# Performance work log

Measured on AMD Instinct MI355X. Metric: run time of the kernel, lower is better.

Reference implementation:

```python
import jax, jax.numpy as jnp
import numpy as np

EPS = 1e-5
D_MODEL = 128; D_INNER = 256; D_STATE = 64; D_CONV = 4; NHEADS = 8; HEADDIM = 32
N_LAYERS = 4; PATCH = 16; IMG = 512; BATCH = 16
D_IN_PROJ = 2 * D_INNER + 2 * D_STATE + NHEADS  # 648
CONV_DIM = D_INNER + 2 * D_STATE               # 384


def _layernorm(x, g, b):
    m = jnp.mean(x, -1, keepdims=True)
    v = jnp.mean((x - m) ** 2, -1, keepdims=True)
    return (x - m) * jax.lax.rsqrt(v + EPS) * g + b


def _mamba2(x, in_w, conv_w, conv_b, dt_bias, A_log, D_skip, norm_w, out_w):
    # x: (b, l, d_model). Faithful to mamba-ssm Mamba2 (ngroups=1, rmsnorm gated, D skip).
    b, l, _ = x.shape
    zxbcdt = jnp.einsum('bld,ed->ble', x, in_w)            # (b,l,648)
    z = zxbcdt[..., :D_INNER]
    xBC = zxbcdt[..., D_INNER:D_INNER + CONV_DIM]
    dt = zxbcdt[..., -NHEADS:]
    # causal depthwise conv1d (kernel D_CONV) + SiLU
    xpad = jnp.pad(xBC, ((0, 0), (D_CONV - 1, 0), (0, 0)))
    xc = conv_b + sum(xpad[:, k:k + l, :] * conv_w[:, k] for k in range(D_CONV))
    xc = jax.nn.silu(xc)
    xs = xc[..., :D_INNER]
    B = xc[..., D_INNER:D_INNER + D_STATE]                 # (b,l,n)
    C = xc[..., -D_STATE:]                                 # (b,l,n)
    dt = jax.nn.softplus(dt + dt_bias)                     # (b,l,h)
    dA = jnp.exp(dt * (-jnp.exp(A_log)))                   # (b,l,h)
    xh = xs.reshape(b, l, NHEADS, HEADDIM)                 # (b,l,h,p)

    def step(hstate, t):
        dA_t, dt_t, B_t, x_t, C_t = t
        hstate = hstate * dA_t[:, :, None, None] + jnp.einsum('bh,bn,bhp->bhpn', dt_t, B_t, x_t)
        return hstate, jnp.einsum('bhpn,bn->bhp', hstate, C_t)

    h0 = jnp.zeros((b, NHEADS, HEADDIM, D_STATE), x.dtype)
    _, ys = jax.lax.scan(step, h0, (dA.swapaxes(0, 1), dt.swapaxes(0, 1), B.swapaxes(0, 1), xh.swapaxes(0, 1), C.swapaxes(0, 1)))
    y = ys.swapaxes(0, 1) + D_skip[None, None, :, None] * xh
    y = y.reshape(b, l, D_INNER)
    y = y * jax.nn.silu(z)                                 # gate
    y = y * jax.lax.rsqrt(jnp.mean(y * y, -1, keepdims=True) + EPS) * norm_w  # gated RMSNorm
    return jnp.einsum('ble,de->bld', y, out_w)


def _forward(x, patch_w, patch_b, pe_g, pe_b, in_w, conv_w, conv_b, dt_bias, A_log,
             D_skip, ssm_norm_w, out_w, ln_g, ln_b, fn_g, fn_b, attn_w1, attn_b1, attn_w2, attn_b2):
    b = x.shape[0]
    Hp = x.shape[2] // PATCH; Wp = x.shape[3] // PATCH
    # patch-embed conv (stride==kernel) as a reshape + einsum
    xp = x.reshape(b, 3, Hp, PATCH, Wp, PATCH)
    tok = jnp.einsum('bchpwq,dcpq->bhwd', xp, patch_w) + patch_b
    tok = tok.reshape(b, Hp * Wp, D_MODEL)
    tok = _layernorm(tok, pe_g, pe_b)
    for i in range(N_LAYERS):
        res = tok
        tok = _layernorm(tok, ln_g[i], ln_b[i])
        tok = _mamba2(tok, in_w[i], conv_w[i], conv_b[i], dt_bias[i], A_log[i],
                      D_skip[i], ssm_norm_w[i], out_w[i])
        tok = tok + res
    tok = _layernorm(tok, fn_g, fn_b)
    # attention pooling
    h1 = jnp.tanh(jnp.einsum('bld,hd->blh', tok, attn_w1) + attn_b1)
    scores = jnp.einsum('blh,oh->blo', h1, attn_w2) + attn_b2
    w = jax.nn.softmax(scores, axis=1)
    pooled = jnp.sum(w * tok, axis=1)
    nrm = jnp.maximum(jnp.sqrt(jnp.sum(pooled * pooled, -1, keepdims=True)), 1e-12)
    return pooled / nrm


def setup_inputs() -> dict:
    key = jax.random.key(0)
    ks = jax.random.split(key, 16)
    n = lambda k, shape, s=0.02: (jax.random.normal(k, shape) * s).astype(jnp.float32)
    return {
        'x': jax.random.normal(ks[0], (BATCH, 3, IMG, IMG), jnp.float32),
        'patch_w': n(ks[1], (D_MODEL, 3, PATCH, PATCH)),
        'patch_b': jnp.zeros((D_MODEL,), jnp.float32),
        'pe_g': jnp.ones((D_MODEL,), jnp.float32),
        'pe_b': jnp.zeros((D_MODEL,), jnp.float32),
        'in_w': n(ks[2], (N_LAYERS, D_IN_PROJ, D_MODEL)),
        'conv_w': n(ks[3], (N_LAYERS, CONV_DIM, D_CONV), 0.1),
        'conv_b': jnp.zeros((N_LAYERS, CONV_DIM), jnp.float32),
        'dt_bias': n(ks[4], (N_LAYERS, NHEADS), 0.5),
        'A_log': jnp.log(jax.random.uniform(ks[5], (N_LAYERS, NHEADS), jnp.float32, 1.0, 16.0)),
        'D_skip': jnp.ones((N_LAYERS, NHEADS), jnp.float32),
        'ssm_norm_w': jnp.ones((N_LAYERS, D_INNER), jnp.float32),
        'out_w': n(ks[6], (N_LAYERS, D_MODEL, D_INNER)),
        'ln_g': jnp.ones((N_LAYERS, D_MODEL), jnp.float32),
        'ln_b': jnp.zeros((N_LAYERS, D_MODEL), jnp.float32),
        'fn_g': jnp.ones((D_MODEL,), jnp.float32),
        'fn_b': jnp.zeros((D_MODEL,), jnp.float32),
        'attn_w1': n(ks[7], (D_MODEL // 2, D_MODEL), 0.05),
        'attn_b1': jnp.zeros((D_MODEL // 2,), jnp.float32),
        'attn_w2': n(ks[8], (1, D_MODEL // 2), 0.05),
        'attn_b2': jnp.zeros((1,), jnp.float32),
    }


def reference(x, patch_w, patch_b, pe_g, pe_b, in_w, conv_w, conv_b, dt_bias, A_log,
              D_skip, ssm_norm_w, out_w, ln_g, ln_b, fn_g, fn_b, attn_w1, attn_b1, attn_w2, attn_b2):
    return _forward(x, patch_w, patch_b, pe_g, pe_b, in_w, conv_w, conv_b, dt_bias, A_log,
                    D_skip, ssm_norm_w, out_w, ln_g, ln_b, fn_g, fn_b, attn_w1, attn_b1, attn_w2, attn_b2)
```

## Files before the change

### kernel.cpp

```cpp
#include <hip/hip_runtime.h>
#include <math.h>

#define EPS 1e-5f

constexpr int NB      = 16;
constexpr int L       = 1024;
constexpr int DM      = 128;
constexpr int DI      = 256;
constexpr int DS      = 64;
constexpr int NH      = 8;
constexpr int DPROJ   = 648;
constexpr int CDIM    = 384;
constexpr int EPAD    = 656;

typedef __attribute__((ext_vector_type(8))) short short8v;
typedef __attribute__((ext_vector_type(4))) float f32x4;
typedef unsigned short ushort_t;

__device__ __forceinline__ float silu_f(float x){ return x / (1.f + expf(-x)); }
__device__ __forceinline__ ushort_t f2bf(float f){
  union { float f; unsigned int u; } v; v.f = f;
  unsigned int r = v.u + 0x7FFF + ((v.u >> 16) & 1);
  return (ushort_t)(r >> 16);
}
__device__ __forceinline__ short8v pack8(float4 a, float4 b){
  short8v v;
  v[0]=(short)f2bf(a.x); v[1]=(short)f2bf(a.y); v[2]=(short)f2bf(a.z); v[3]=(short)f2bf(a.w);
  v[4]=(short)f2bf(b.x); v[5]=(short)f2bf(b.y); v[6]=(short)f2bf(b.z); v[7]=(short)f2bf(b.w);
  return v;
}

__global__ __launch_bounds__(256) void k_cvt(const float* __restrict__ in_w,
    const float* __restrict__ ln_g, const float* __restrict__ ln_b,
    const float* __restrict__ out_w, const float* __restrict__ nw,
    const float* __restrict__ patch_w, const float* __restrict__ w1,
    ushort_t* __restrict__ inwb, ushort_t* __restrict__ owb,
    ushort_t* __restrict__ pwb, float* __restrict__ biasin,
    ushort_t* __restrict__ w1b){
  const int R1 = 4 * EPAD * 128, R2 = 4 * 128 * 256, R3 = 128 * 768, R4 = 4 * EPAD, R5 = 64 * 128;
  int i = blockIdx.x * 256 + threadIdx.x;
  if (i < R1) {
    int ly = i / (EPAD * 128), rem = i % (EPAD * 128), e = rem >> 7, d = rem & 127;
    float v = 0.f;
    if (e < DPROJ) v = in_w[((size_t)ly * DPROJ + e) * 128 + d] * ln_g[ly * 128 + d];
    inwb[i] = f2bf(v);
    return;
  }
  i -= R1;
  if (i < R2) {
    int ly = i >> 15, rem = i & 32767, e = rem & 255;
    owb[i] = f2bf(out_w[i] * nw[ly * 256 + e]);
    return;
  }
  i -= R2;
  if (i < R3) { pwb[i] = f2bf(patch_w[i]); return; }
  i -= R3;
  if (i < R4) {
    int ly = i / EPAD, e = i % EPAD;
    float s = 0.f;
    if (e < DPROJ) {
      const float* r = in_w + ((size_t)ly * DPROJ + e) * 128;
      const float* b = ln_b + ly * 128;
      for (int d = 0; d < 128; ++d) s += r[d] * b[d];
    }
    biasin[i] = s;
    return;
  }
  i -= R4;
  if (i < R5) w1b[i] = f2bf(w1[i]);
}

__global__ __launch_bounds__(256) void k_patch(const float* __restrict__ x,
    const ushort_t* __restrict__ pwb, const float* __restrict__ pb,
    const float* __restrict__ pg, const float* __restrict__ pbe,
    float* __restrict__ tok){
  __shared__ ushort_t Al[64 * 128];
  __shared__ ushort_t Bl[128 * 128];
  __shared__ float spb[128], spg[128], spe[128];
  const int m0 = blockIdx.x * 64;
  const int tid = threadIdx.x;
  char* Ab = (char*)Al; char* Bb = (char*)Bl;
  if (tid < 128) { spb[tid] = pb[tid]; spg[tid] = pg[tid]; spe[tid] = pbe[tid]; }
  const int w = tid >> 6, l = tid & 63, lr = l & 15, lgp = l >> 4;
  f32x4 acc[8];
#pragma unroll
  for (int nt = 0; nt < 8; ++nt) acc[nt] = (f32x4){0.f, 0.f, 0.f, 0.f};
  for (int kc = 0; kc < 6; ++kc) {
    __syncthreads();
    for (int idx = tid; idx < 128 * 16; idx += 256) {
      int n = idx >> 4, ch = idx & 15;
      short8v v = *(const short8v*)(pwb + (size_t)n * 768 + kc * 128 + (ch << 3));
      *(short8v*)(Bb + n * 256 + ((ch * 16) ^ ((n & 7) << 4))) = v;
    }
    {
      const int c = kc >> 1;
      for (int i = tid; i < 1024; i += 256) {
        int t = i >> 4, p = (i >> 1) & 7, o = i & 1;
        int T = m0 + t, bb = T >> 10, tl = T & 1023, hp = tl >> 5, wp = tl & 31;
        const float* src = x + (((size_t)(bb * 3 + c) * 512 + hp * 16 + ((kc & 1) << 3) + p) * 512
                                + wp * 16 + o * 8);
        float4 f0 = *(const float4*)src;
        float4 f1 = *(const float4*)(src + 4);
        short8v v = pack8(f0, f1);
        int kk = p * 16 + o * 8;
        *(short8v*)(Ab + t * 256 + ((kk * 2) ^ ((t & 7) << 4))) = v;
      }
    }
    __syncthreads();
    short8v a[4];
#pragma unroll
    for (int ks = 0; ks < 4; ++ks)
      a[ks] = *(const short8v*)(Ab + (16 * w + lr) * 256 + ((ks * 64 + lgp * 16) ^ ((lr & 7) << 4)));
#pragma unroll
    for (int nt = 0; nt < 8; ++nt) {
#pragma unroll
      for (int ks = 0; ks < 4; ++ks) {
        short8v b = *(const short8v*)(Bb + (nt * 16 + lr) * 256 + ((ks * 64 + lgp * 16) ^ ((lr & 7) << 4)));
        acc[nt] = __builtin_amdgcn_mfma_f32_16x16x32_bf16(a[ks], b, acc[nt], 0, 0, 0);
      }
    }
  }
  float s4[4] = {0,0,0,0}, q4[4] = {0,0,0,0};
#pragma unroll
  for (int nt = 0; nt < 8; ++nt) {
    const float bb = spb[nt * 16 + lr];
#pragma unroll
    for (int r = 0; r < 4; ++r) { float v = acc[nt][r] + bb; s4[r] += v; q4[r] += v * v; }
  }
#pragma unroll
  for (int r = 0; r < 4; ++r) {
    for (int off = 1; off < 16; off <<= 1) {
      s4[r] += __shfl_xor(s4[r], off, 16);
      q4[r] += __shfl_xor(q4[r], off, 16);
    }
  }
#pragma unroll
  for (int r = 0; r < 4; ++r) {
    float mean = s4[r] * (1.f / 128.f);
    float var  = q4[r] * (1.f / 128.f) - mean * mean;
    float rstd = rsqrtf(var + EPS);
    const size_t row = (size_t)(m0 + 16 * w + lgp * 4 + r) * 128;
#pragma unroll
    for (int nt = 0; nt < 8; ++nt) {
      int col = nt * 16 + lr;
      float v = acc[nt][r] + spb[col];
      tok[row + col] = (v - mean) * rstd * spg[col] + spe[col];
    }
  }
}

__global__ __launch_bounds__(256) void k_inproj(const float* __restrict__ tok,
    const ushort_t* __restrict__ inwb, const float* __restrict__ biasin,
    float* __restrict__ zx){
  __shared__ ushort_t Al[128 * 128];
  __shared__ ushort_t Bl[176 * 128];
  __shared__ float sBias[176];
  const int blk = blockIdx.x;
  const int mb = blk >> 2, nb = blk & 3;
  const int m0 = mb << 7, n0 = nb * 176;
  const int NT = (nb == 3) ? 128 : 176;
  const int tid = threadIdx.x;
  char* Ab = (char*)Al; char* Bb = (char*)Bl;
  for (int idx = tid; idx < (NT << 4); idx += 256) {
    int row = idx >> 4, ch = idx & 15;
    short8v v = *(const short8v*)(inwb + ((size_t)(n0 + row) << 7) + (ch << 3));
    *(short8v*)(Bb + row * 256 + ((ch * 16) ^ ((row & 7) << 4))) = v;
  }
  for (int idx = tid; idx < NT; idx += 256) sBias[idx] = biasin[n0 + idx];
  for (int rp = 0; rp < 2; ++rp) {
    const int r = (rp << 6) + (tid >> 2), t4 = tid & 3;
    const float* src = tok + (((size_t)(m0 + r)) << 7) + t4 * 32;
    float v[32];
    float s = 0.f, sq = 0.f;
#pragma unroll
    for (int k = 0; k < 8; ++k) {
      float4 f = *(const float4*)(src + 4 * k);
      v[4*k] = f.x; v[4*k+1] = f.y; v[4*k+2] = f.z; v[4*k+3] = f.w;
      s += f.x + f.y + f.z + f.w;
      sq += f.x*f.x + f.y*f.y + f.z*f.z + f.w*f.w;
    }
    s  += __shfl_xor(s, 1, 4);  s  += __shfl_xor(s, 2, 4);
    sq += __shfl_xor(sq, 1, 4); sq += __shfl_xor(sq, 2, 4);
    float mean = s * (1.f / 128.f);
    float var  = sq * (1.f / 128.f) - mean * mean;
    float rstd = rsqrtf(var + EPS);
#pragma unroll
    for (int k = 0; k < 4; ++k) {
      short8v o;
#pragma unroll
      for (int e = 0; e < 8; ++e) o[e] = (short)f2bf((v[8*k + e] - mean) * rstd);
      *(short8v*)(Ab + r * 256 + ((t4 * 64 + 16 * k) ^ ((r & 7) << 4))) = o;
    }
  }
  __syncthreads();
  const int w = tid >> 6, l = tid & 63, lr = l & 15, lgp = l >> 4;
  const int xsl = (lr & 7) << 4;
  short8v a[2][4];
#pragma unroll
  for (int mi = 0; mi < 2; ++mi) {
    const int mt = w + mi * 4;
#pragma unroll
    for (int ks = 0; ks < 4; ++ks)
      a[mi][ks] = *(const short8v*)(Ab + (16 * mt + lr) * 256 + ((ks * 64 + lgp * 16) ^ xsl));
  }
  const int NTT = NT >> 4;
  for (int nt = 0; nt < NTT; ++nt) {
    f32x4 acc0 = (f32x4){0.f, 0.f, 0.f, 0.f};
    f32x4 acc1 = (f32x4){0.f, 0.f, 0.f, 0.f};
#pragma unroll
    for (int ks = 0; ks < 4; ++ks) {
      short8v b = *(const short8v*)(Bb + (nt * 16 + lr) * 256 + ((ks * 64 + lgp * 16) ^ xsl));
      acc0 = __builtin_amdgcn_mfma_f32_16x16x32_bf16(a[0][ks], b, acc0, 0, 0, 0);
      acc1 = __builtin_amdgcn_mfma_f32_16x16x32_bf16(a[1][ks], b, acc1, 0, 0, 0);
    }
    const int col = n0 + nt * 16 + lr;
    if (col < DPROJ) {
      const float bias = sBias[nt * 16 + lr];
#pragma unroll
      for (int r = 0; r < 4; ++r) {
        zx[((size_t)(m0 + 16 * w       + lgp * 4 + r)) * DPROJ + col] = acc0[r] + bias;
        zx[((size_t)(m0 + 16 * (w + 4) + lgp * 4 + r)) * DPROJ + col] = acc1[r] + bias;
      }
    }
  }
}

constexpr int CONVC = 192;
__global__ __launch_bounds__(256) void k_conv(const float* __restrict__ zx,
    const float* __restrict__ cw, const float* __restrict__ cb, float* __restrict__ xc){
  __shared__ float st[67][CONVC];
  __shared__ float swt[CONVC][4];
  __shared__ float sbias[CONVC];
  const int blk = blockIdx.x;
  const int cg = blk & 1, tile = (blk >> 1) & 15, b = blk >> 5;
  const int l0 = tile << 6, ch0 = cg * CONVC;
  const int tid = threadIdx.x;
  for (int i = tid; i < CONVC; i += 256) {
    float4 wv = *(const float4*)(cw + (size_t)(ch0 + i) * 4);
    swt[i][0] = wv.x; swt[i][1] = wv.y; swt[i][2] = wv.z; swt[i][3] = wv.w;
    sbias[i] = cb[ch0 + i];
  }
  for (int i = tid; i < 67 * 48; i += 256) {
    int rr = i / 48, q4 = i % 48;
    int lrow = l0 + rr - 3;
    float4 v = make_float4(0.f, 0.f, 0.f, 0.f);
    if (lrow >= 0) v = *(const float4*)(zx + ((size_t)(b << 10) + lrow) * DPROJ + DI + ch0 + q4 * 4);
    *(float4*)(&st[rr][q4 * 4]) = v;
  }
  __syncthreads();
  for (int i = tid; i < 64 * CONVC; i += 256) {
    int t = i / CONVC, c2 = i % CONVC;
    float acc = sbias[c2] + st[t][c2] * swt[c2][0] + st[t+1][c2] * swt[c2][1]
              + st[t+2][c2] * swt[c2][2] + st[t+3][c2] * swt[c2][3];
    acc = silu_f(acc);
    xc[((size_t)(b << 10) + l0 + t) * CDIM + ch0 + c2] = acc;
  }
}

__global__ __launch_bounds__(64) void k_dt(const float* __restrict__ zx,
    const float* __restrict__ dtbias, const float* __restrict__ Alog,
    float* __restrict__ dtb, float* __restrict__ lcb, float* __restrict__ Acb){
  const int blk = blockIdx.x;
  const int c = blk & 15, h = (blk >> 4) & 7, b = blk >> 7;
  const int s = threadIdx.x;
  const int l = (c << 6) + s;
  float raw = zx[((size_t)(b << 10) + l) * DPROJ + 640 + h] + dtbias[h];
  float dt = raw > 20.f ? raw : log1pf(expf(raw));
  float la = dt * (-expf(Alog[h]));
  float cum = la;
  for (int off = 1; off < 64; off <<= 1) {
    float v = __shfl_up(cum, off, 64);
    if (s >= off) cum += v;
  }
  size_t o = ((size_t)((b << 3) + h) << 10) + l;
  dtb[o] = dt; lcb[o] = cum;
  if (s == 63) Acb[blk] = expf(cum);
}

__global__ __launch_bounds__(256) void k_cstate(const float* __restrict__ xc,
    const float* __restrict__ dtb, const float* __restrict__ lcb,
    float* __restrict__ Sc){
  __shared__ ushort_t sXc[32 * 64];
  __shared__ ushort_t sBt[64 * 64];
  __shared__ float scoef[64];
  const int blk = blockIdx.x;
  const int c = blk & 15, h = (blk >> 4) & 7, b = blk >> 7;
  const int tid = threadIdx.x;
  const int l0 = c << 6;
  char* pA = (char*)sXc; char* pB = (char*)sBt;
  const size_t obh = ((size_t)((b << 3) + h) << 10) + l0;
  if (tid < 64) {
    float lcT = lcb[obh + 63];
    scoef[tid] = dtb[obh + tid] * __expf(fminf(lcT - lcb[obh + tid], 0.f));
  }
  const int s = tid >> 2, q = tid & 3;
  const size_t rowb = ((size_t)(b << 10) + l0 + s) * CDIM;
  float4 b0 = *(const float4*)(xc + rowb + DI + q * 16);
  float4 b1 = *(const float4*)(xc + rowb + DI + q * 16 + 4);
  float4 b2 = *(const float4*)(xc + rowb + DI + q * 16 + 8);
  float4 b3 = *(const float4*)(xc + rowb + DI + q * 16 + 12);
  float4 x0 = *(const float4*)(xc + rowb + (h << 5) + q * 8);
  float4 x1 = *(const float4*)(xc + rowb + (h << 5) + q * 8 + 4);
  float bv[16] = {b0.x,b0.y,b0.z,b0.w, b1.x,b1.y,b1.z,b1.w,
                  b2.x,b2.y,b2.z,b2.w, b3.x,b3.y,b3.z,b3.w};
#pragma unroll
  for (int j = 0; j < 16; ++j) {
    const int n = q * 16 + j;
    *(ushort_t*)(pB + n * 128 + ((s * 2) ^ ((n & 7) << 4))) = f2bf(bv[j]);
  }
  __syncthreads();
  const float cf = scoef[s];
  float xv[8] = {x0.x,x0.y,x0.z,x0.w, x1.x,x1.y,x1.z,x1.w};
#pragma unroll
  for (int j = 0; j < 8; ++j) {
    const int p = q * 8 + j;
    *(ushort_t*)(pA + p * 128 + ((s * 2) ^ ((p & 7) << 4))) = f2bf(cf * xv[j]);
  }
  __syncthreads();
  const int w = tid >> 6, l = tid & 63, lr = l & 15, lgp = l >> 4;
  const int xsl = (lr & 7) << 4;
  const int pt = w & 1, ng = w >> 1;
  short8v a0 = *(const short8v*)(pA + (pt * 16 + lr) * 128 + ((lgp * 16) ^ xsl));
  short8v a1 = *(const short8v*)(pA + (pt * 16 + lr) * 128 + ((64 + lgp * 16) ^ xsl));
  float* dst = Sc + ((size_t)blk << 11);
#pragma unroll
  for (int ni = 0; ni < 2; ++ni) {
    const int nt = ng * 2 + ni;
    f32x4 acc = (f32x4){0.f, 0.f, 0.f, 0.f};
    short8v bb0 = *(const short8v*)(pB + (nt * 16 + lr) * 128 + ((lgp * 16) ^ xsl));
    short8v bb1 = *(const short8v*)(pB + (nt * 16 + lr) * 128 + ((64 + lgp * 16) ^ xsl));
    acc = __builtin_amdgcn_mfma_f32_16x16x32_bf16(a0, bb0, acc, 0, 0, 0);
    acc = __builtin_amdgcn_mfma_f32_16x16x32_bf16(a1, bb1, acc, 0, 0, 0);
#pragma unroll
    for (int r = 0; r < 4; ++r)
      dst[(pt * 16 + lgp * 4 + r) * 64 + nt * 16 + lr] = acc[r];
  }
}

__global__ __launch_bounds__(256) void k_hscan(float* __restrict__ Sc, const float* __restrict__ Acb){
  const int blk = blockIdx.x;
  const int bh = blk >> 3;
  const int e = ((blk & 7) << 8) + threadIdx.x;
  float hs = 0.f;
  const size_t base = ((size_t)bh << 15) + e;
  for (int c = 0; c < 16; ++c) {
    const size_t o = base + ((size_t)c << 11);
    float v = Sc[o];
    Sc[o] = hs;
    hs = Acb[(bh << 4) + c] * hs + v;
  }
}

__global__ __launch_bounds__(256) void k_chunky(const float* __restrict__ xc,
    const float* __restrict__ h0buf, const float* __restrict__ dtb,
    const float* __restrict__ lcb, const float* __restrict__ Dsk,
    float* __restrict__ ys){
  __shared__ ushort_t sC[64 * 64];
  __shared__ ushort_t sBm[64 * 64];
  __shared__ ushort_t sAW[64 * 128];
  __shared__ ushort_t sBX[32 * 128];
  __shared__ float sXT[32][65];
  __shared__ float sdt[64], slc[64];
  const int blk = blockIdx.x;
  const int c = blk & 15, h = (blk >> 4) & 7, b = blk >> 7;
  const int tid = threadIdx.x;
  const int l0 = c << 6;
  char* pC = (char*)sC; char* pB = (char*)sBm; char* pA = (char*)sAW; char* pX = (char*)sBX;
  const size_t obh = ((size_t)((b << 3) + h) << 10) + l0;
  if (tid < 64) { sdt[tid] = dtb[obh + tid]; slc[tid] = lcb[obh + tid]; }
  {
    const int row = tid >> 2, q = tid & 3;
    const size_t rowb = ((size_t)(b << 10) + l0 + row) * CDIM;
    const float Pt = __expf(lcb[obh + row]);
    const int xs = (row & 7) << 4;
    float4 b0 = *(const float4*)(xc + rowb + DI + q * 16);
    float4 b1 = *(const float4*)(xc + rowb + DI + q * 16 + 4);
    float4 b2 = *(const float4*)(xc + rowb + DI + q * 16 + 8);
    float4 b3 = *(const float4*)(xc + rowb + DI + q * 16 + 12);
    *(short8v*)(pB + row * 128 + ((q * 32) ^ xs))      = pack8(b0, b1);
    *(short8v*)(pB + row * 128 + ((q * 32 + 16) ^ xs)) = pack8(b2, b3);
    float4 c0 = *(const float4*)(xc + rowb + DI + DS + q * 16);
    float4 c1 = *(const float4*)(xc + rowb + DI + DS + q * 16 + 4);
    float4 c2 = *(const float4*)(xc + rowb + DI + DS + q * 16 + 8);
    float4 c3 = *(const float4*)(xc + rowb + DI + DS + q * 16 + 12);
    *(short8v*)(pC + row * 128 + ((q * 32) ^ xs))      = pack8(c0, c1);
    *(short8v*)(pC + row * 128 + ((q * 32 + 16) ^ xs)) = pack8(c2, c3);
    float4 p0 = make_float4(c0.x*Pt, c0.y*Pt, c0.z*Pt, c0.w*Pt);
    float4 p1 = make_float4(c1.x*Pt, c1.y*Pt, c1.z*Pt, c1.w*Pt);
    float4 p2 = make_float4(c2.x*Pt, c2.y*Pt, c2.z*Pt, c2.w*Pt);
    float4 p3 = make_float4(c3.x*Pt, c3.y*Pt, c3.z*Pt, c3.w*Pt);
    *(short8v*)(pA + row * 256 + ((128 + q * 32) ^ xs))      = pack8(p0, p1);
    *(short8v*)(pA + row * 256 + ((128 + q * 32 + 16) ^ xs)) = pack8(p2, p3);
    float4 x0 = *(const float4*)(xc + rowb + (h << 5) + q * 8);
    float4 x1 = *(const float4*)(xc + rowb + (h << 5) + q * 8 + 4);
    sXT[q*8+0][row] = x0.x; sXT[q*8+1][row] = x0.y; sXT[q*8+2][row] = x0.z; sXT[q*8+3][row] = x0.w;
    sXT[q*8+4][row] = x1.x; sXT[q*8+5][row] = x1.y; sXT[q*8+6][row] = x1.z; sXT[q*8+7][row] = x1.w;
  }
  {
    const int p = tid >> 3, n8 = (tid & 7) << 3;
    float4 h0a = *(const float4*)(h0buf + ((size_t)blk << 11) + (p << 6) + n8);
    float4 h0b = *(const float4*)(h0buf + ((size_t)blk << 11) + (p << 6) + n8 + 4);
    *(short8v*)(pX + p * 256 + (((64 + n8) * 2) ^ ((p & 7) << 4))) = pack8(h0a, h0b);
  }
  __syncthreads();
  {
    const int p = tid >> 3, s8 = (tid & 7) << 3;
    short8v vx;
#pragma unroll
    for (int e = 0; e < 8; ++e) vx[e] = (short)f2bf(sXT[p][s8 + e]);
    *(short8v*)(pX + p * 256 + ((s8 * 2) ^ ((p & 7) << 4))) = vx;
  }
  const int w = tid >> 6, l = tid & 63, lr = l & 15, lgp = l >> 4;
  const int xsl = (lr & 7) << 4;
  f32x4 accg[4];
#pragma unroll
  for (int nt = 0; nt < 4; ++nt) accg[nt] = (f32x4){0.f, 0.f, 0.f, 0.f};
  {
    short8v a0 = *(const short8v*)(pC + (16 * w + lr) * 128 + ((lgp * 16) ^ xsl));
    short8v a1 = *(const short8v*)(pC + (16 * w + lr) * 128 + ((64 + lgp * 16) ^ xsl));
#pragma unroll
    for (int nt = 0; nt < 4; ++nt) {
      short8v b0 = *(const short8v*)(pB + (nt * 16 + lr) * 128 + ((lgp * 16) ^ xsl));
      short8v b1 = *(const short8v*)(pB + (nt * 16 + lr) * 128 + ((64 + lgp * 16) ^ xsl));
      accg[nt] = __builtin_amdgcn_mfma_f32_16x16x32_bf16(a0, b0, accg[nt], 0, 0, 0);
      accg[nt] = __builtin_amdgcn_mfma_f32_16x16x32_bf16(a1, b1, accg[nt], 0, 0, 0);
    }
  }
#pragma unroll
  for (int nt = 0; nt < 4; ++nt) {
    const int s = nt * 16 + lr;
    const float ds = sdt[s], ls = slc[s];
#pragma unroll
    for (int r = 0; r < 4; ++r) {
      const int t = 16 * w + lgp * 4 + r;
      float wv = 0.f;
      if (s <= t) wv = ds * __expf(fminf(slc[t] - ls, 0.f)) * accg[nt][r];
      *(ushort_t*)(pA + t * 256 + ((s * 2) ^ ((t & 7) << 4))) = f2bf(wv);
    }
  }
  __syncthreads();
  f32x4 accy[2];
  accy[0] = (f32x4){0.f, 0.f, 0.f, 0.f};
  accy[1] = (f32x4){0.f, 0.f, 0.f, 0.f};
  short8v aw[4];
#pragma unroll
  for (int ks = 0; ks < 4; ++ks)
    aw[ks] = *(const short8v*)(pA + (16 * w + lr) * 256 + ((ks * 64 + lgp * 16) ^ xsl));
#pragma unroll
  for (int nt = 0; nt < 2; ++nt) {
#pragma unroll
    for (int ks = 0; ks < 4; ++ks) {
      short8v bx = *(const short8v*)(pX + (nt * 16 + lr) * 256 + ((ks * 64 + lgp * 16) ^ xsl));
      accy[nt] = __builtin_amdgcn_mfma_f32_16x16x32_bf16(aw[ks], bx, accy[nt], 0, 0, 0);
    }
  }
  const float dsk = Dsk[h];
#pragma unroll
  for (int nt = 0; nt < 2; ++nt) {
    const int p = nt * 16 + lr;
#pragma unroll
    for (int r = 0; r < 4; ++r) {
      const int t = 16 * w + lgp * 4 + r;
      ys[((size_t)(b << 10) + l0 + t) * DI + (h << 5) + p] = accy[nt][r] + dsk * sXT[p][t];
    }
  }
}

__global__ __launch_bounds__(256) void k_gateout(const float* __restrict__ zx,
    const float* __restrict__ ys, const ushort_t* __restrict__ owb,
    float* __restrict__ tok){
  __shared__ ushort_t Al[64 * 256];
  __shared__ ushort_t Bl[128 * 64];
  const int m0 = blockIdx.x * 64;
  const int tid = threadIdx.x;
  char* Ab = (char*)Al; char* Bb = (char*)Bl;
  {
    const int r = tid >> 2, t4 = tid & 3;
    const size_t row = (size_t)(m0 + r);
    const float* yp = ys + row * 256 + t4 * 64;
    const float* zp = zx + row * DPROJ + t4 * 64;
    float p[64];
    float sq = 0.f;
#pragma unroll
    for (int k = 0; k < 16; ++k) {
      float4 fy = *(const float4*)(yp + 4 * k);
      float4 fz = *(const float4*)(zp + 4 * k);
      float a0 = fy.x * (fz.x / (1.f + __expf(-fz.x)));
      float a1 = fy.y * (fz.y / (1.f + __expf(-fz.y)));
      float a2 = fy.z * (fz.z / (1.f + __expf(-fz.z)));
      float a3 = fy.w * (fz.w / (1.f + __expf(-fz.w)));
      p[4*k] = a0; p[4*k+1] = a1; p[4*k+2] = a2; p[4*k+3] = a3;
      sq += a0*a0 + a1*a1 + a2*a2 + a3*a3;
    }
    sq += __shfl_xor(sq, 1, 4); sq += __shfl_xor(sq, 2, 4);
    float rstd = rsqrtf(sq * (1.f / 256.f) + EPS);
#pragma unroll
    for (int k = 0; k < 8; ++k) {
      short8v o;
#pragma unroll
      for (int e = 0; e < 8; ++e) o[e] = (short)f2bf(p[8*k + e] * rstd);
      *(short8v*)(Ab + r * 512 + ((t4 * 128 + 16 * k) ^ ((r & 7) << 4))) = o;
    }
  }
  const int w = tid >> 6, l = tid & 63, lr = l & 15, lgp = l >> 4;
  f32x4 acc[8];
#pragma unroll
  for (int nt = 0; nt < 8; ++nt) acc[nt] = (f32x4){0.f, 0.f, 0.f, 0.f};
  for (int kq = 0; kq < 4; ++kq) {
    __syncthreads();
    for (int idx = tid; idx < 128 * 8; idx += 256) {
      int row = idx >> 3, ch = idx & 7;
      short8v v = *(const short8v*)(owb + ((size_t)row << 8) + kq * 64 + (ch << 3));
      *(short8v*)(Bb + row * 128 + ((ch * 16) ^ ((row & 7) << 4))) = v;
    }
    __syncthreads();
    short8v a0 = *(const short8v*)(Ab + (16*w + lr) * 512 + ((kq * 128 +      lgp * 16) ^ ((lr & 7) << 4)));
    short8v a1 = *(const short8v*)(Ab + (16*w + lr) * 512 + ((kq * 128 + 64 + lgp * 16) ^ ((lr & 7) << 4)));
#pragma unroll
    for (int nt = 0; nt < 8; ++nt) {
      short8v b0 = *(const short8v*)(Bb + (nt * 16 + lr) * 128 + ((     lgp * 16) ^ ((lr & 7) << 4)));
      short8v b1 = *(const short8v*)(Bb + (nt * 16 + lr) * 128 + ((64 + lgp * 16) ^ ((lr & 7) << 4)));
      acc[nt] = __builtin_amdgcn_mfma_f32_16x16x32_bf16(a0, b0, acc[nt], 0, 0, 0);
      acc[nt] = __builtin_amdgcn_mfma_f32_16x16x32_bf16(a1, b1, acc[nt], 0, 0, 0);
    }
  }
#pragma unroll
  for (int nt = 0; nt < 8; ++nt) {
#pragma unroll
    for (int r = 0; r < 4; ++r) {
      tok[((size_t)(m0 + 16 * w + lgp * 4 + r)) * 128 + nt * 16 + lr] += acc[nt][r];
    }
  }
}

__global__ __launch_bounds__(256) void k_score(const float* __restrict__ tok,
    const float* __restrict__ fg, const float* __restrict__ fb,
    const ushort_t* __restrict__ w1b, const float* __restrict__ b1,
    const float* __restrict__ w2, const float* __restrict__ b2,
    float* __restrict__ tokF, float* __restrict__ sc){
  __shared__ ushort_t Al[64 * 128];
  __shared__ ushort_t Wl[64 * 128];
  __shared__ float sb1[64], sw2[64];
  const int m0 = blockIdx.x * 64;
  const int tid = threadIdx.x;
  char* Ab = (char*)Al; char* Wb = (char*)Wl;
  for (int idx = tid; idx < 64 * 16; idx += 256) {
    int row = idx >> 4, ch = idx & 15;
    short8v v = *(const short8v*)(w1b + (row << 7) + (ch << 3));
    *(short8v*)(Wb + row * 256 + ((ch * 16) ^ ((row & 7) << 4))) = v;
  }
  if (tid < 64) { sb1[tid] = b1[tid]; sw2[tid] = w2[tid]; }
  {
    const int r = tid >> 2, t4 = tid & 3;
    const float* src = tok + (((size_t)(m0 + r)) << 7) + t4 * 32;
    float v[32];
    float s = 0.f, sq = 0.f;
#pragma unroll
    for (int k = 0; k < 8; ++k) {
      float4 f = *(const float4*)(src + 4 * k);
      v[4*k] = f.x; v[4*k+1] = f.y; v[4*k+2] = f.z; v[4*k+3] = f.w;
      s += f.x + f.y + f.z + f.w;
      sq += f.x*f.x + f.y*f.y + f.z*f.z + f.w*f.w;
    }
    s  += __shfl_xor(s, 1, 4);  s  += __shfl_xor(s, 2, 4);
    sq += __shfl_xor(sq, 1, 4); sq += __shfl_xor(sq, 2, 4);
    float mean = s * (1.f / 128.f);
    float var  = sq * (1.f / 128.f) - mean * mean;
    float rstd = rsqrtf(var + EPS);
    float* tdst = tokF + (((size_t)(m0 + r)) << 7) + t4 * 32;
#pragma unroll
    for (int k = 0; k < 4; ++k) {
      float o8[8];
      float4 g0 = *(const float4*)(fg + t4 * 32 + 8 * k);
      float4 g1 = *(const float4*)(fg + t4 * 32 + 8 * k + 4);
      float4 e0 = *(const float4*)(fb + t4 * 32 + 8 * k);
      float4 e1 = *(const float4*)(fb + t4 * 32 + 8 * k + 4);
      o8[0] = (v[8*k+0]-mean)*rstd*g0.x + e0.x; o8[1] = (v[8*k+1]-mean)*rstd*g0.y + e0.y;
      o8[2] = (v[8*k+2]-mean)*rstd*g0.z + e0.z; o8[3] = (v[8*k+3]-mean)*rstd*g0.w + e0.w;
      o8[4] = (v[8*k+4]-mean)*rstd*g1.x + e1.x; o8[5] = (v[8*k+5]-mean)*rstd*g1.y + e1.y;
      o8[6] = (v[8*k+6]-mean)*rstd*g1.z + e1.z; o8[7] = (v[8*k+7]-mean)*rstd*g1.w + e1.w;
      *(float4*)(tdst + 8*k)     = make_float4(o8[0], o8[1], o8[2], o8[3]);
      *(float4*)(tdst + 8*k + 4) = make_float4(o8[4], o8[5], o8[6], o8[7]);
      short8v ov;
#pragma unroll
      for (int e = 0; e < 8; ++e) ov[e] = (short)f2bf(o8[e]);
      *(short8v*)(Ab + r * 256 + ((t4 * 64 + 16 * k) ^ ((r & 7) << 4))) = ov;
    }
  }
  __syncthreads();
  const int w = tid >> 6, l = tid & 63, lr = l & 15, lgp = l >> 4;
  const int xsl = (lr & 7) << 4;
  short8v a[4];
#pragma unroll
  for (int ks = 0; ks < 4; ++ks)
    a[ks] = *(const short8v*)(Ab + (16 * w + lr) * 256 + ((ks * 64 + lgp * 16) ^ xsl));
  float sacc[4] = {0.f, 0.f, 0.f, 0.f};
#pragma unroll
  for (int nt = 0; nt < 4; ++nt) {
    f32x4 acc = (f32x4){0.f, 0.f, 0.f, 0.f};
#pragma unroll
    for (int ks = 0; ks < 4; ++ks) {
      short8v bb = *(const short8v*)(Wb + (nt * 16 + lr) * 256 + ((ks * 64 + lgp * 16) ^ xsl));
      acc = __builtin_amdgcn_mfma_f32_16x16x32_bf16(a[ks], bb, acc, 0, 0, 0);
    }
    const float bias = sb1[nt * 16 + lr], wv = sw2[nt * 16 + lr];
#pragma unroll
    for (int r = 0; r < 4; ++r) sacc[r] += tanhf(acc[r] + bias) * wv;
  }
#pragma unroll
  for (int r = 0; r < 4; ++r) {
    for (int off = 1; off < 16; off <<= 1) sacc[r] += __shfl_xor(sacc[r], off, 16);
  }
  if (lr == 0) {
    const float bb2 = b2[0];
#pragma unroll
    for (int r = 0; r < 4; ++r) sc[m0 + 16 * w + lgp * 4 + r] = sacc[r] + bb2;
  }
}

__global__ __launch_bounds__(256) void k_pool1(const float* __restrict__ tokF,
    const float* __restrict__ sc, float* __restrict__ pp){
  __shared__ float sw[128];
  __shared__ float sacc[128];
  __shared__ float sse[2];
  const int bs = blockIdx.x, b = bs >> 3, seg = bs & 7, tid = threadIdx.x;
  const int l0 = (b << 10) + (seg << 7);
  if (tid < 128) sw[tid] = __expf(sc[l0 + tid]);
  __syncthreads();
  const int d = tid & 127, g = tid >> 7;
  const float* tf = tokF + ((size_t)(l0 + (g << 6))) * 128 + d;
  float acc = 0.f;
#pragma unroll 4
  for (int i = 0; i < 64; ++i) acc += sw[(g << 6) + i] * tf[(size_t)i * 128];
  if (g == 0) sacc[d] = acc;
  float e = (tid < 128) ? sw[tid] : 0.f;
  for (int off = 32; off; off >>= 1) e += __shfl_xor(e, off);
  if ((tid & 63) == 0 && tid < 128) sse[tid >> 6] = e;
  __syncthreads();
  if (g == 1) pp[bs * 132 + d] = sacc[d] + acc;
  if (tid == 0) pp[bs * 132 + 128] = sse[0] + sse[1];
}

__global__ __launch_bounds__(128) void k_pool2(const float* __restrict__ pp,
    float* __restrict__ out){
  __shared__ float s2[2];
  const int b = blockIdx.x, tid = threadIdx.x;
  float num = 0.f, den = 0.f;
#pragma unroll
  for (int seg = 0; seg < 8; ++seg) {
    num += pp[(b * 8 + seg) * 132 + tid];
    den += pp[(b * 8 + seg) * 132 + 128];
  }
  float pooled = num / den;
  float sq = pooled * pooled;
  for (int off = 32; off; off >>= 1) sq += __shfl_xor(sq, off);
  if ((tid & 63) == 0) s2[tid >> 6] = sq;
  __syncthreads();
  float nrm = fmaxf(sqrtf(s2[0] + s2[1]), 1e-12f);
  out[(size_t)b * 128 + tid] = pooled / nrm;
}

extern "C" void kernel_launch(void* const* d_in, const int* in_sizes, int n_in,
                              void* d_out, int out_size, void* d_ws, size_t ws_size,
                              hipStream_t stream) {
  const float* x       = (const float*)d_in[0];
  const float* patch_w = (const float*)d_in[1];
  const float* patch_b = (const float*)d_in[2];
  const float* pe_g    = (const float*)d_in[3];
  const float* pe_b    = (const float*)d_in[4];
  const float* in_w    = (const float*)d_in[5];
  const float* conv_w  = (const float*)d_in[6];
  const float* conv_b  = (const float*)d_in[7];
  const float* dt_bias = (const float*)d_in[8];
  const float* A_log   = (const float*)d_in[9];
  const float* D_skip  = (const float*)d_in[10];
  const float* nw      = (const float*)d_in[11];
  const float* out_w   = (const float*)d_in[12];
  const float* ln_g    = (const float*)d_in[13];
  const float* ln_b    = (const float*)d_in[14];
  const float* fn_g    = (const float*)d_in[15];
  const float* fn_b    = (const float*)d_in[16];
  const float* w1      = (const float*)d_in[17];
  const float* b1      = (const float*)d_in[18];
  const float* w2      = (const float*)d_in[19];
  const float* b2      = (const float*)d_in[20];
  float* out = (float*)d_out;
  char* ws = (char*)d_ws;

  size_t off = 0;
  float* tok  = (float*)(ws + off); off += (size_t)NB * L * DM * 4;
  float* zx   = (float*)(ws + off); off += (size_t)NB * L * DPROJ * 4;
  float* xcb  = (float*)(ws + off); off += (size_t)NB * L * CDIM * 4;
  float* ysb  = (float*)(ws + off); off += (size_t)NB * L * DI * 4;
  float* Scb  = (float*)(ws + off); off += (size_t)NB * NH * 16 * 2048 * 4;
  float* dtb  = (float*)(ws + off); off += (size_t)NB * NH * L * 4;
  float* lcb  = (float*)(ws + off); off += (size_t)NB * NH * L * 4;
  float* Acb  = (float*)(ws + off); off += (size_t)NB * NH * 16 * 4;
  ushort_t* inwb = (ushort_t*)(ws + off); off += (size_t)4 * EPAD * 128 * 2;
  ushort_t* owb  = (ushort_t*)(ws + off); off += (size_t)4 * 128 * 256 * 2;
  ushort_t* pwb  = (ushort_t*)(ws + off); off += (size_t)128 * 768 * 2;
  float* biasin  = (float*)(ws + off); off += (size_t)4 * EPAD * 4;
  ushort_t* w1b  = (ushort_t*)(ws + off); off += (size_t)64 * 128 * 2;
  float* pp      = (float*)(ws + off); off += (size_t)128 * 132 * 4;
  float* tokF = zx;
  float* scb  = (float*)(ws + (size_t)30 * 1024 * 1024);

  {
    const int total = 4 * EPAD * 128 + 4 * 128 * 256 + 128 * 768 + 4 * EPAD + 64 * 128;
    k_cvt<<<(total + 255) / 256, 256, 0, stream>>>(in_w, ln_g, ln_b, out_w, nw, patch_w, w1,
                                                   inwb, owb, pwb, biasin, w1b);
  }
  k_patch<<<256, 256, 0, stream>>>(x, pwb, patch_b, pe_g, pe_b, tok);
  for (int ly = 0; ly < 4; ++ly) {
    k_inproj<<<512, 256, 0, stream>>>(tok, inwb + (size_t)ly * EPAD * 128,
                                      biasin + ly * EPAD, zx);
    k_conv<<<NB * 16 * 2, 256, 0, stream>>>(zx, conv_w + (size_t)ly * CDIM * 4,
                                            conv_b + ly * CDIM, xcb);
    k_dt<<<NB * NH * 16, 64, 0, stream>>>(zx, dt_bias + ly * NH, A_log + ly * NH,
                                          dtb, lcb, Acb);
    k_cstate<<<NB * NH * 16, 256, 0, stream>>>(xcb, dtb, lcb, Scb);
    k_hscan<<<NB * NH * 8, 256, 0, stream>>>(Scb, Acb);
    k_chunky<<<NB * NH * 16, 256, 0, stream>>>(xcb, Scb, dtb, lcb,
                                               D_skip + ly * NH, ysb);
    k_gateout<<<256, 256, 0, stream>>>(zx, ysb, owb + (size_t)ly * 128 * 256, tok);
  }
  k_score<<<256, 256, 0, stream>>>(tok, fn_g, fn_b, w1b, b1, w2, b2, tokF, scb);
  k_pool1<<<128, 256, 0, stream>>>(tokF, scb, pp);
  k_pool2<<<16, 128, 0, stream>>>(pp, out);
}
```

Before: 513.8 us.

## Store conv output and SSM output as bf16; fuse dt scan into conv kernel

The conv output (xc) and chunked-scan output (ys) buffers are now stored as bf16 instead of fp32, which halves their global memory traffic. Downstream kernels (cstate, chunky, gateout) read them as packed short8 vectors and convert where needed. The separate dt/softplus/cumsum kernel is folded into the conv kernel, so one launch per layer goes away. In exchange, precision is lower: xc is rounded to bf16 earlier, and the D-skip term plus the gate inputs now see bf16-rounded values.

```diff
diff --git a/kernel.cpp b/kernel.cpp
--- a/kernel.cpp
+++ b/kernel.cpp
@@ -14,6 +14,7 @@
 constexpr int EPAD    = 656;
 
 typedef __attribute__((ext_vector_type(8))) short short8v;
+typedef __attribute__((ext_vector_type(4))) short short4v;
 typedef __attribute__((ext_vector_type(4))) float f32x4;
 typedef unsigned short ushort_t;
 
@@ -22,6 +23,10 @@
   union { float f; unsigned int u; } v; v.f = f;
   unsigned int r = v.u + 0x7FFF + ((v.u >> 16) & 1);
   return (ushort_t)(r >> 16);
+}
+__device__ __forceinline__ float bf2f(ushort_t u){
+  union { float f; unsigned int u; } v; v.u = ((unsigned int)u) << 16;
+  return v.f;
 }
 __device__ __forceinline__ short8v pack8(float4 a, float4 b){
   short8v v;
@@ -227,7 +232,10 @@
 
 constexpr int CONVC = 192;
 __global__ __launch_bounds__(256) void k_conv(const float* __restrict__ zx,
-    const float* __restrict__ cw, const float* __restrict__ cb, float* __restrict__ xc){
+    const float* __restrict__ cw, const float* __restrict__ cb,
+    const float* __restrict__ dtbias, const float* __restrict__ Alog,
+    ushort_t* __restrict__ xc, float* __restrict__ dtb,
+    float* __restrict__ lcb, float* __restrict__ Acb){
   __shared__ float st[67][CONVC];
   __shared__ float swt[CONVC][4];
   __shared__ float sbias[CONVC];
@@ -247,37 +255,39 @@
     if (lrow >= 0) v = *(const float4*)(zx + ((size_t)(b << 10) + lrow) * DPROJ + DI + ch0 + q4 * 4);
     *(float4*)(&st[rr][q4 * 4]) = v;
   }
-  __syncthreads();
-  for (int i = tid; i < 64 * CONVC; i += 256) {
-    int t = i / CONVC, c2 = i % CONVC;
-    float acc = sbias[c2] + st[t][c2] * swt[c2][0] + st[t+1][c2] * swt[c2][1]
-              + st[t+2][c2] * swt[c2][2] + st[t+3][c2] * swt[c2][3];
-    acc = silu_f(acc);
-    xc[((size_t)(b << 10) + l0 + t) * CDIM + ch0 + c2] = acc;
-  }
-}
-
-__global__ __launch_bounds__(64) void k_dt(const float* __restrict__ zx,
-    const float* __restrict__ dtbias, const float* __restrict__ Alog,
-    float* __restrict__ dtb, float* __restrict__ lcb, float* __restrict__ Acb){
-  const int blk = blockIdx.x;
-  const int c = blk & 15, h = (blk >> 4) & 7, b = blk >> 7;
-  const int s = threadIdx.x;
-  const int l = (c << 6) + s;
-  float raw = zx[((size_t)(b << 10) + l) * DPROJ + 640 + h] + dtbias[h];
-  float dt = raw > 20.f ? raw : log1pf(expf(raw));
-  float la = dt * (-expf(Alog[h]));
-  float cum = la;
-  for (int off = 1; off < 64; off <<= 1) {
-    float v = __shfl_up(cum, off, 64);
-    if (s >= off) cum += v;
-  }
-  size_t o = ((size_t)((b << 3) + h) << 10) + l;
-  dtb[o] = dt; lcb[o] = cum;
-  if (s == 63) Acb[blk] = expf(cum);
-}
-
-__global__ __launch_bounds__(256) void k_cstate(const float* __restrict__ xc,
+  if (cg == 0) {
+    const int wv = tid >> 6, lane = tid & 63;
+#pragma unroll
+    for (int i = 0; i < 2; ++i) {
+      const int hh = wv * 2 + i;
+      float raw = zx[((size_t)(b << 10) + l0 + lane) * DPROJ + 640 + hh] + dtbias[hh];
+      float dt = raw > 20.f ? raw : log1pf(expf(raw));
+      float cum = dt * (-expf(Alog[hh]));
+      for (int off = 1; off < 64; off <<= 1) {
+        float v = __shfl_up(cum, off, 64);
+        if (lane >= off) cum += v;
+      }
+      size_t o = ((size_t)((b << 3) + hh) << 10) + l0 + lane;
+      dtb[o] = dt; lcb[o] = cum;
+      if (lane == 63) Acb[((b << 3) + hh) * 16 + tile] = expf(cum);
+    }
+  }
+  __syncthreads();
+  for (int i = tid; i < 64 * 48; i += 256) {
+    int t = i / 48, g = i % 48;
+    short4v ov;
+#pragma unroll
+    for (int j = 0; j < 4; ++j) {
+      int c2 = g * 4 + j;
+      float acc = sbias[c2] + st[t][c2] * swt[c2][0] + st[t+1][c2] * swt[c2][1]
+                + st[t+2][c2] * swt[c2][2] + st[t+3][c2] * swt[c2][3];
+      ov[j] = (short)f2bf(silu_f(acc));
+    }
+    *(short4v*)(xc + ((size_t)(b << 10) + l0 + t) * CDIM + ch0 + g * 4) = ov;
+  }
+}
+
+__global__ __launch_bounds__(256) void k_cstate(const ushort_t* __restrict__ xc,
     const float* __restrict__ dtb, const float* __restrict__ lcb,
     float* __restrict__ Sc){
   __shared__ ushort_t sXc[32 * 64];
@@ -294,27 +304,22 @@
     scoef[tid] = dtb[obh + tid] * __expf(fminf(lcT - lcb[obh + tid], 0.f));
   }
   const int s = tid >> 2, q = tid & 3;
-  const size_t rowb = ((size_t)(b << 10) + l0 + s) * CDIM;
-  float4 b0 = *(const float4*)(xc + rowb + DI + q * 16);
-  float4 b1 = *(const float4*)(xc + rowb + DI + q * 16 + 4);
-  float4 b2 = *(const float4*)(xc + rowb + DI + q * 16 + 8);
-  float4 b3 = *(const float4*)(xc + rowb + DI + q * 16 + 12);
-  float4 x0 = *(const float4*)(xc + rowb + (h << 5) + q * 8);
-  float4 x1 = *(const float4*)(xc + rowb + (h << 5) + q * 8 + 4);
-  float bv[16] = {b0.x,b0.y,b0.z,b0.w, b1.x,b1.y,b1.z,b1.w,
-                  b2.x,b2.y,b2.z,b2.w, b3.x,b3.y,b3.z,b3.w};
+  const ushort_t* xr = xc + ((size_t)(b << 10) + l0 + s) * CDIM;
+  short8v b0 = *(const short8v*)(xr + 256 + q * 16);
+  short8v b1 = *(const short8v*)(xr + 256 + q * 16 + 8);
+  short8v x8 = *(const short8v*)(xr + (h << 5) + q * 8);
 #pragma unroll
   for (int j = 0; j < 16; ++j) {
     const int n = q * 16 + j;
-    *(ushort_t*)(pB + n * 128 + ((s * 2) ^ ((n & 7) << 4))) = f2bf(bv[j]);
+    ushort_t bv = (ushort_t)(j < 8 ? b0[j] : b1[j - 8]);
+    *(ushort_t*)(pB + n * 128 + ((s * 2) ^ ((n & 7) << 4))) = bv;
   }
   __syncthreads();
   const float cf = scoef[s];
-  float xv[8] = {x0.x,x0.y,x0.z,x0.w, x1.x,x1.y,x1.z,x1.w};
 #pragma unroll
   for (int j = 0; j < 8; ++j) {
     const int p = q * 8 + j;
-    *(ushort_t*)(pA + p * 128 + ((s * 2) ^ ((p & 7) << 4))) = f2bf(cf * xv[j]);
+    *(ushort_t*)(pA + p * 128 + ((s * 2) ^ ((p & 7) << 4))) = f2bf(cf * bf2f((ushort_t)x8[j]));
   }
   __syncthreads();
   const int w = tid >> 6, l = tid & 63, lr = l & 15, lgp = l >> 4;
@@ -351,10 +356,10 @@
   }
 }
 
-__global__ __launch_bounds__(256) void k_chunky(const float* __restrict__ xc,
+__global__ __launch_bounds__(256) void k_chunky(const ushort_t* __restrict__ xc,
     const float* __restrict__ h0buf, const float* __restrict__ dtb,
     const float* __restrict__ lcb, const float* __restrict__ Dsk,
-    float* __restrict__ ys){
+    ushort_t* __restrict__ ys){
   __shared__ ushort_t sC[64 * 64];
   __shared__ ushort_t sBm[64 * 64];
   __shared__ ushort_t sAW[64 * 128];
@@ -370,31 +375,28 @@
   if (tid < 64) { sdt[tid] = dtb[obh + tid]; slc[tid] = lcb[obh + tid]; }
   {
     const int row = tid >> 2, q = tid & 3;
-    const size_t rowb = ((size_t)(b << 10) + l0 + row) * CDIM;
+    const ushort_t* xr = xc + ((size_t)(b << 10) + l0 + row) * CDIM;
+    const int xs = (row & 7) << 4;
+    short8v b0 = *(const short8v*)(xr + 256 + q * 16);
+    short8v b1 = *(const short8v*)(xr + 256 + q * 16 + 8);
+    *(short8v*)(pB + row * 128 + ((q * 32) ^ xs))      = b0;
+    *(short8v*)(pB + row * 128 + ((q * 32 + 16) ^ xs)) = b1;
+    short8v c0 = *(const short8v*)(xr + 320 + q * 16);
+    short8v c1 = *(const short8v*)(xr + 320 + q * 16 + 8);
+    *(short8v*)(pC + row * 128 + ((q * 32) ^ xs))      = c0;
+    *(short8v*)(pC + row * 128 + ((q * 32 + 16) ^ xs)) = c1;
     const float Pt = __expf(lcb[obh + row]);
-    const int xs = (row & 7) << 4;
-    float4 b0 = *(const float4*)(xc + rowb + DI + q * 16);
-    float4 b1 = *(const float4*)(xc + rowb + DI + q * 16 + 4);
-    float4 b2 = *(const float4*)(xc + rowb + DI + q * 16 + 8);
-    float4 b3 = *(const float4*)(xc + rowb + DI + q * 16 + 12);
-    *(short8v*)(pB + row * 128 + ((q * 32) ^ xs))      = pack8(b0, b1);
-    *(short8v*)(pB + row * 128 + ((q * 32 + 16) ^ xs)) = pack8(b2, b3);
-    float4 c0 = *(const float4*)(xc + rowb + DI + DS + q * 16);
-    float4 c1 = *(const float4*)(xc + rowb + DI + DS + q * 16 + 4);
-    float4 c2 = *(const float4*)(xc + rowb + DI + DS + q * 16 + 8);
-    float4 c3 = *(const float4*)(xc + rowb + DI + DS + q * 16 + 12);
-    *(short8v*)(pC + row * 128 + ((q * 32) ^ xs))      = pack8(c0, c1);
-    *(short8v*)(pC + row * 128 + ((q * 32 + 16) ^ xs)) = pack8(c2, c3);
-    float4 p0 = make_float4(c0.x*Pt, c0.y*Pt, c0.z*Pt, c0.w*Pt);
-    float4 p1 = make_float4(c1.x*Pt, c1.y*Pt, c1.z*Pt, c1.w*Pt);
-    float4 p2 = make_float4(c2.x*Pt, c2.y*Pt, c2.z*Pt, c2.w*Pt);
-    float4 p3 = make_float4(c3.x*Pt, c3.y*Pt, c3.z*Pt, c3.w*Pt);
-    *(short8v*)(pA + row * 256 + ((128 + q * 32) ^ xs))      = pack8(p0, p1);
-    *(short8v*)(pA + row * 256 + ((128 + q * 32 + 16) ^ xs)) = pack8(p2, p3);
-    float4 x0 = *(const float4*)(xc + rowb + (h << 5) + q * 8);
-    float4 x1 = *(const float4*)(xc + rowb + (h << 5) + q * 8 + 4);
-    sXT[q*8+0][row] = x0.x; sXT[q*8+1][row] = x0.y; sXT[q*8+2][row] = x0.z; sXT[q*8+3][row] = x0.w;
-    sXT[q*8+4][row] = x1.x; sXT[q*8+5][row] = x1.y; sXT[q*8+6][row] = x1.z; sXT[q*8+7][row] = x1.w;
+    short8v q0, q1;
+#pragma unroll
+    for (int j = 0; j < 8; ++j) {
+      q0[j] = (short)f2bf(Pt * bf2f((ushort_t)c0[j]));
+      q1[j] = (short)f2bf(Pt * bf2f((ushort_t)c1[j]));
+    }
+    *(short8v*)(pA + row * 256 + ((128 + q * 32) ^ xs))      = q0;
+    *(short8v*)(pA + row * 256 + ((128 + q * 32 + 16) ^ xs)) = q1;
+    short8v x8 = *(const short8v*)(xr + (h << 5) + q * 8);
+#pragma unroll
+    for (int j = 0; j < 8; ++j) sXT[q * 8 + j][row] = bf2f((ushort_t)x8[j]);
   }
   {
     const int p = tid >> 3, n8 = (tid & 7) << 3;
@@ -461,13 +463,13 @@
 #pragma unroll
     for (int r = 0; r < 4; ++r) {
       const int t = 16 * w + lgp * 4 + r;
-      ys[((size_t)(b << 10) + l0 + t) * DI + (h << 5) + p] = accy[nt][r] + dsk * sXT[p][t];
+      ys[((size_t)(b << 10) + l0 + t) * DI + (h << 5) + p] = f2bf(accy[nt][r] + dsk * sXT[p][t]);
     }
   }
 }
 
 __global__ __launch_bounds__(256) void k_gateout(const float* __restrict__ zx,
-    const float* __restrict__ ys, const ushort_t* __restrict__ owb,
+    const ushort_t* __restrict__ ysb, const ushort_t* __restrict__ owb,
     float* __restrict__ tok){
   __shared__ ushort_t Al[64 * 256];
   __shared__ ushort_t Bl[128 * 64];
@@ -477,20 +479,21 @@
   {
     const int r = tid >> 2, t4 = tid & 3;
     const size_t row = (size_t)(m0 + r);
-    const float* yp = ys + row * 256 + t4 * 64;
+    const ushort_t* yp = ysb + row * 256 + t4 * 64;
     const float* zp = zx + row * DPROJ + t4 * 64;
     float p[64];
     float sq = 0.f;
 #pragma unroll
-    for (int k = 0; k < 16; ++k) {
-      float4 fy = *(const float4*)(yp + 4 * k);
-      float4 fz = *(const float4*)(zp + 4 * k);
-      float a0 = fy.x * (fz.x / (1.f + __expf(-fz.x)));
-      float a1 = fy.y * (fz.y / (1.f + __expf(-fz.y)));
-      float a2 = fy.z * (fz.z / (1.f + __expf(-fz.z)));
-      float a3 = fy.w * (fz.w / (1.f + __expf(-fz.w)));
-      p[4*k] = a0; p[4*k+1] = a1; p[4*k+2] = a2; p[4*k+3] = a3;
-      sq += a0*a0 + a1*a1 + a2*a2 + a3*a3;
+    for (int k = 0; k < 8; ++k) {
+      short8v y8 = *(const short8v*)(yp + 8 * k);
+      float4 fz0 = *(const float4*)(zp + 8 * k);
+      float4 fz1 = *(const float4*)(zp + 8 * k + 4);
+      float zz[8] = {fz0.x, fz0.y, fz0.z, fz0.w, fz1.x, fz1.y, fz1.z, fz1.w};
+#pragma unroll
+      for (int j = 0; j < 8; ++j) {
+        float a = bf2f((ushort_t)y8[j]) * (zz[j] / (1.f + __expf(-zz[j])));
+        p[8 * k + j] = a; sq += a * a;
+      }
     }
     sq += __shfl_xor(sq, 1, 4); sq += __shfl_xor(sq, 2, 4);
     float rstd = rsqrtf(sq * (1.f / 256.f) + EPS);
@@ -690,8 +693,8 @@
   size_t off = 0;
   float* tok  = (float*)(ws + off); off += (size_t)NB * L * DM * 4;
   float* zx   = (float*)(ws + off); off += (size_t)NB * L * DPROJ * 4;
-  float* xcb  = (float*)(ws + off); off += (size_t)NB * L * CDIM * 4;
-  float* ysb  = (float*)(ws + off); off += (size_t)NB * L * DI * 4;
+  ushort_t* xcb = (ushort_t*)(ws + off); off += (size_t)NB * L * CDIM * 2;
+  ushort_t* ysb = (ushort_t*)(ws + off); off += (size_t)NB * L * DI * 2;
   float* Scb  = (float*)(ws + off); off += (size_t)NB * NH * 16 * 2048 * 4;
   float* dtb  = (float*)(ws + off); off += (size_t)NB * NH * L * 4;
   float* lcb  = (float*)(ws + off); off += (size_t)NB * NH * L * 4;
@@ -715,9 +718,8 @@
     k_inproj<<<512, 256, 0, stream>>>(tok, inwb + (size_t)ly * EPAD * 128,
                                       biasin + ly * EPAD, zx);
     k_conv<<<NB * 16 * 2, 256, 0, stream>>>(zx, conv_w + (size_t)ly * CDIM * 4,
-                                            conv_b + ly * CDIM, xcb);
-    k_dt<<<NB * NH * 16, 64, 0, stream>>>(zx, dt_bias + ly * NH, A_log + ly * NH,
-                                          dtb, lcb, Acb);
+                                            conv_b + ly * CDIM, dt_bias + ly * NH,
+                                            A_log + ly * NH, xcb, dtb, lcb, Acb);
     k_cstate<<<NB * NH * 16, 256, 0, stream>>>(xcb, dtb, lcb, Scb);
     k_hscan<<<NB * NH * 8, 256, 0, stream>>>(Scb, Acb);
     k_chunky<<<NB * NH * 16, 256, 0, stream>>>(xcb, Scb, dtb, lcb,
```

Measured after the change: 478.5 us. -6.9%, faster.
